# Kernel tuning notes

Hardware: AMD Instinct MI355X
Metric: run time of the kernel (lower is better)

Reference implementation:

```python
import jax, jax.numpy as jnp
import numpy as np

LEAKY_SLOPE = 0.2  # tf.nn.leaky_relu default alpha


def setup_inputs() -> dict:
    key = jax.random.key(0)
    k1, k2, k3 = jax.random.split(key, 3)
    B, T, K, D = 64, 2048, 256, 256  # batch, timesteps, n_nodes, out_dim
    inputs = jax.random.normal(k1, (B, T, K), dtype=jnp.float32)
    W = jax.random.normal(k2, (K, D), dtype=jnp.float32) * (1.0 / np.sqrt(K))
    a = jax.random.normal(k3, (2 * D, 1), dtype=jnp.float32) * (1.0 / np.sqrt(2 * D))
    return {"inputs": inputs, "W": W, "a": a}


def reference(inputs, W, a):
    # inputs: (B, T, K); W: (K, D); a: (2D, 1)
    B, T, K = inputs.shape
    D = W.shape[1]
    H = jnp.matmul(inputs, W)  # (B, T, D)
    # Original: H_concat[b,t,k] = concat([H[b,t], H[b,t]]) for every k (both
    # repeats are of the same H), so H_concat @ a == H @ (a_i + a_j), constant in k.
    a_i = a[:D, 0]
    a_j = a[D:, 0]
    e = jax.nn.leaky_relu(H @ (a_i + a_j), negative_slope=LEAKY_SLOPE)  # (B, T)
    e = jnp.broadcast_to(e[:, :, None], (B, T, K))  # (B, T, K) -- constant along K
    alpha = jax.nn.softmax(e, axis=2)  # exactly uniform 1/K
    # sum_k alpha[b,t,k] * H[b,t,d]  (H_repeat_i[b,t,k,:] == H[b,t,:])
    H_gat = jnp.einsum('btk,btd->btd', alpha, H)  # (B, T, D)
    return H_gat
```

## Files before the change

kernel.cpp:

```cpp
#include <hip/hip_runtime.h>
#include <cstdint>


static constexpr int MTOT = 64 * 2048;
static constexpr int KDIM = 256;
static constexpr int NDIM = 256;

typedef __bf16 bf16x8 __attribute__((ext_vector_type(8)));
typedef float f32x4 __attribute__((ext_vector_type(4)));

__device__ __forceinline__ uint32_t f2bf_pk(float a, float b) {
    uint32_t ua = __float_as_uint(a);
    uint32_t ub = __float_as_uint(b);
    ua = ua + 0x7fffu + ((ua >> 16) & 1u);
    ub = ub + 0x7fffu + ((ub >> 16) & 1u);
    return (ua >> 16) | (ub & 0xffff0000u);
}

__global__ void wt_transpose(const float* __restrict__ W, unsigned short* __restrict__ Wt) {
    int n = blockIdx.x;
    int k = threadIdx.x;
    float v = W[k * NDIM + n];
    uint32_t u = __float_as_uint(v);
    u = u + 0x7fffu + ((u >> 16) & 1u);
    Wt[n * KDIM + k] = (unsigned short)(u >> 16);
}

__global__ __launch_bounds__(1024, 1)
void gat_gemm(const float* __restrict__ A, const unsigned short* __restrict__ Wt,
              float* __restrict__ C) {
    __shared__ alignas(16) unsigned short Bs[128 * 256];
    __shared__ alignas(16) unsigned short As[2][256 * 64];

    const int tid  = threadIdx.x;
    const int lane = tid & 63;
    const int wave = tid >> 6;
    const int l15  = lane & 15;
    const int quad = lane >> 4;
    const int wm   = wave & 7;
    const int wn   = wave >> 3;

    const int b     = blockIdx.x;
    const int nhalf = (b >> 3) & 1;
    const int mt    = (b & 7) | ((b >> 4) << 3);
    const int bm    = mt * 256;
    const int bn    = nhalf * 128;

    const int arow = tid >> 4;
    const int acol = (tid & 15) * 4;
    const int as8  = (tid & 15) * 8;

    f32x4 acc[2][4];
#pragma unroll
    for (int i = 0; i < 2; ++i)
#pragma unroll
        for (int j = 0; j < 4; ++j)
            acc[i][j] = (f32x4)0.0f;

    auto issueA = [&](int kt, float4 (&R)[4]) {
#pragma unroll
        for (int i = 0; i < 4; ++i)
            R[i] = *(const float4*)(A + (size_t)(bm + i * 64 + arow) * KDIM + kt * 64 + acol);
    };
    auto writeA = [&](unsigned short* dst, float4 (&R)[4]) {
#pragma unroll
        for (int i = 0; i < 4; ++i) {
            const int r = i * 64 + arow;
            uint2 w;
            w.x = f2bf_pk(R[i].x, R[i].y);
            w.y = f2bf_pk(R[i].z, R[i].w);
            *(uint2*)((char*)dst + r * 128 + (as8 ^ ((r & 7) << 4))) = w;
        }
    };
    auto compute = [&](const unsigned short* asrc, int kt) {
        const char* asb = (const char*)asrc;
#pragma unroll
        for (int ks = 0; ks < 2; ++ks) {
            bf16x8 af[2];
#pragma unroll
            for (int i = 0; i < 2; ++i) {
                const int row = wm * 32 + i * 16 + l15;
                af[i] = *(const bf16x8*)(asb + row * 128 +
                          ((ks * 64 + quad * 16) ^ ((row & 7) << 4)));
            }
#pragma unroll
            for (int j = 0; j < 4; ++j) {
                const int n = wn * 64 + j * 16 + l15;
                bf16x8 bf = *(const bf16x8*)((const char*)Bs + n * 512 +
                              ((kt * 128 + ks * 64 + quad * 16) ^ ((n & 7) << 4)));
#pragma unroll
                for (int i = 0; i < 2; ++i)
                    acc[i][j] = __builtin_amdgcn_mfma_f32_16x16x32_bf16(af[i], bf, acc[i][j], 0, 0, 0);
            }
        }
    };
    auto wavebar = [&]() {
        asm volatile("s_waitcnt lgkmcnt(0)" ::: "memory");
        __builtin_amdgcn_s_barrier();
        asm volatile("" ::: "memory");
    };

    uint4 bv[4];
#pragma unroll
    for (int c = 0; c < 4; ++c) {
        const int idx = c * 1024 + tid;
        bv[c] = *(const uint4*)(Wt + (size_t)(bn + (idx >> 5)) * KDIM + (idx & 31) * 8);
    }
    float4 R0[4], R1[4];
    issueA(0, R0);
    issueA(1, R1);
#pragma unroll
    for (int c = 0; c < 4; ++c) {
        const int idx = c * 1024 + tid;
        const int n = idx >> 5, kc = idx & 31;
        *(uint4*)((char*)Bs + n * 512 + ((kc * 16) ^ ((n & 7) << 4))) = bv[c];
    }
    writeA(&As[0][0], R0);
    wavebar();

#pragma unroll
    for (int kt = 0; kt < 4; ++kt) {
        if (kt < 2) {
            if ((kt & 1) == 0) issueA(kt + 2, R0); else issueA(kt + 2, R1);
        }
        compute(&As[kt & 1][0], kt);
        if (kt < 3) {
            if ((kt & 1) == 0) writeA(&As[1][0], R1); else writeA(&As[0][0], R0);
            wavebar();
        }
    }

#pragma unroll
    for (int i = 0; i < 2; ++i) {
#pragma unroll
        for (int r = 0; r < 4; ++r) {
            const size_t row = (size_t)(bm + wm * 32 + i * 16 + quad * 4 + r);
            float* cp = C + row * NDIM + bn + wn * 64 + l15;
#pragma unroll
            for (int j = 0; j < 4; ++j)
                cp[j * 16] = acc[i][j][r];
        }
    }
}

extern "C" void kernel_launch(void* const* d_in, const int* in_sizes, int n_in,
                              void* d_out, int out_size, void* d_ws, size_t ws_size,
                              hipStream_t stream) {
    (void)in_sizes; (void)n_in; (void)out_size; (void)ws_size;
    const float* inputs = (const float*)d_in[0];
    const float* W      = (const float*)d_in[1];
    unsigned short* Wt = (unsigned short*)d_ws;
    float* out = (float*)d_out;

    hipLaunchKernelGGL(wt_transpose, dim3(NDIM), dim3(KDIM), 0, stream, W, Wt);
    hipLaunchKernelGGL(gat_gemm, dim3((MTOT / 256) * 2), dim3(1024), 0, stream, inputs, Wt, out);
}
```

Baseline: 237.0 us.

## Keep full W in LDS and stream 512 rows per block over 4 subtiles

Each block now loads the entire bf16 W (256x256) into shared memory once and loops over four 128-row M subtiles, each covering the full N width, writing results after each subtile. Before, every 256x128 tile reloaded its half of W and the A rows were read once per N half. This removes the duplicate reads of A and cuts repeated W loads. In exchange, A uses a single LDS buffer with two barriers per k-step, and the grid shrinks to 256 blocks.

```diff
diff --git a/kernel.cpp b/kernel.cpp
--- a/kernel.cpp
+++ b/kernel.cpp
@@ -29,22 +29,18 @@
 __global__ __launch_bounds__(1024, 1)
 void gat_gemm(const float* __restrict__ A, const unsigned short* __restrict__ Wt,
               float* __restrict__ C) {
-    __shared__ alignas(16) unsigned short Bs[128 * 256];
-    __shared__ alignas(16) unsigned short As[2][256 * 64];
+    __shared__ alignas(16) unsigned short Bs[256 * 256];
+    __shared__ alignas(16) unsigned short As[128 * 64];
 
     const int tid  = threadIdx.x;
     const int lane = tid & 63;
     const int wave = tid >> 6;
     const int l15  = lane & 15;
     const int quad = lane >> 4;
-    const int wm   = wave & 7;
-    const int wn   = wave >> 3;
+    const int wm   = wave & 3;
+    const int wn   = wave >> 2;
 
-    const int b     = blockIdx.x;
-    const int nhalf = (b >> 3) & 1;
-    const int mt    = (b & 7) | ((b >> 4) << 3);
-    const int bm    = mt * 256;
-    const int bn    = nhalf * 128;
+    const size_t bbase = (size_t)blockIdx.x * 512;
 
     const int arow = tid >> 4;
     const int acol = (tid & 15) * 4;
@@ -57,30 +53,27 @@
         for (int j = 0; j < 4; ++j)
             acc[i][j] = (f32x4)0.0f;
 
-    auto issueA = [&](int kt, float4 (&R)[4]) {
-#pragma unroll
-        for (int i = 0; i < 4; ++i)
-            R[i] = *(const float4*)(A + (size_t)(bm + i * 64 + arow) * KDIM + kt * 64 + acol);
+    auto issueA = [&](int s, float4 (&R)[2]) {
+        const float* ap = A + (bbase + (size_t)(s >> 2) * 128) * KDIM + (s & 3) * 64 + acol;
+        R[0] = *(const float4*)(ap + (size_t)arow * KDIM);
+        R[1] = *(const float4*)(ap + (size_t)(arow + 64) * KDIM);
     };
-    auto writeA = [&](unsigned short* dst, float4 (&R)[4]) {
-#pragma unroll
-        for (int i = 0; i < 4; ++i) {
-            const int r = i * 64 + arow;
-            uint2 w;
-            w.x = f2bf_pk(R[i].x, R[i].y);
-            w.y = f2bf_pk(R[i].z, R[i].w);
-            *(uint2*)((char*)dst + r * 128 + (as8 ^ ((r & 7) << 4))) = w;
-        }
+    auto writeA = [&](float4 (&R)[2]) {
+        uint2 w0, w1;
+        w0.x = f2bf_pk(R[0].x, R[0].y); w0.y = f2bf_pk(R[0].z, R[0].w);
+        w1.x = f2bf_pk(R[1].x, R[1].y); w1.y = f2bf_pk(R[1].z, R[1].w);
+        const int r0 = arow, r1 = arow + 64;
+        *(uint2*)((char*)As + r0 * 128 + (as8 ^ ((r0 & 7) << 4))) = w0;
+        *(uint2*)((char*)As + r1 * 128 + (as8 ^ ((r1 & 7) << 4))) = w1;
     };
-    auto compute = [&](const unsigned short* asrc, int kt) {
-        const char* asb = (const char*)asrc;
+    auto compute = [&](int kt) {
 #pragma unroll
         for (int ks = 0; ks < 2; ++ks) {
             bf16x8 af[2];
 #pragma unroll
             for (int i = 0; i < 2; ++i) {
                 const int row = wm * 32 + i * 16 + l15;
-                af[i] = *(const bf16x8*)(asb + row * 128 +
+                af[i] = *(const bf16x8*)((const char*)As + row * 128 +
                           ((ks * 64 + quad * 16) ^ ((row & 7) << 4)));
             }
 #pragma unroll
@@ -100,45 +93,54 @@
         asm volatile("" ::: "memory");
     };
 
-    uint4 bv[4];
+    uint4 bv[8];
 #pragma unroll
-    for (int c = 0; c < 4; ++c) {
+    for (int c = 0; c < 8; ++c) {
         const int idx = c * 1024 + tid;
-        bv[c] = *(const uint4*)(Wt + (size_t)(bn + (idx >> 5)) * KDIM + (idx & 31) * 8);
+        bv[c] = *(const uint4*)(Wt + (size_t)(idx >> 5) * KDIM + (idx & 31) * 8);
     }
-    float4 R0[4], R1[4];
+    float4 R0[2], R1[2];
     issueA(0, R0);
     issueA(1, R1);
 #pragma unroll
-    for (int c = 0; c < 4; ++c) {
+    for (int c = 0; c < 8; ++c) {
         const int idx = c * 1024 + tid;
         const int n = idx >> 5, kc = idx & 31;
         *(uint4*)((char*)Bs + n * 512 + ((kc * 16) ^ ((n & 7) << 4))) = bv[c];
     }
-    writeA(&As[0][0], R0);
+    writeA(R0);
     wavebar();
 
 #pragma unroll
-    for (int kt = 0; kt < 4; ++kt) {
-        if (kt < 2) {
-            if ((kt & 1) == 0) issueA(kt + 2, R0); else issueA(kt + 2, R1);
+    for (int s = 0; s < 16; ++s) {
+        if (s < 14) {
+            if (s & 1) issueA(s + 2, R1); else issueA(s + 2, R0);
         }
-        compute(&As[kt & 1][0], kt);
-        if (kt < 3) {
-            if ((kt & 1) == 0) writeA(&As[1][0], R1); else writeA(&As[0][0], R0);
+        compute(s & 3);
+
+        if ((s & 3) == 3) {
+            const size_t mb = bbase + (size_t)(s >> 2) * 128 + wm * 32;
+#pragma unroll
+            for (int i = 0; i < 2; ++i) {
+#pragma unroll
+                for (int r = 0; r < 4; ++r) {
+                    float* cp = C + (mb + i * 16 + quad * 4 + r) * NDIM + wn * 64 + l15;
+#pragma unroll
+                    for (int j = 0; j < 4; ++j)
+                        cp[j * 16] = acc[i][j][r];
+                }
+            }
+#pragma unroll
+            for (int i = 0; i < 2; ++i)
+#pragma unroll
+                for (int j = 0; j < 4; ++j)
+                    acc[i][j] = (f32x4)0.0f;
+        }
+
+        if (s < 15) {
             wavebar();
-        }
-    }
-
-#pragma unroll
-    for (int i = 0; i < 2; ++i) {
-#pragma unroll
-        for (int r = 0; r < 4; ++r) {
-            const size_t row = (size_t)(bm + wm * 32 + i * 16 + quad * 4 + r);
-            float* cp = C + row * NDIM + bn + wn * 64 + l15;
-#pragma unroll
-            for (int j = 0; j < 4; ++j)
-                cp[j * 16] = acc[i][j][r];
+            if (s & 1) writeA(R0); else writeA(R1);
+            wavebar();
         }
     }
 }
@@ -153,5 +155,5 @@
     float* out = (float*)d_out;
 
     hipLaunchKernelGGL(wt_transpose, dim3(NDIM), dim3(KDIM), 0, stream, W, Wt);
-    hipLaunchKernelGGL(gat_gemm, dim3((MTOT / 256) * 2), dim3(1024), 0, stream, inputs, Wt, out);
+    hipLaunchKernelGGL(gat_gemm, dim3(MTOT / 512), dim3(1024), 0, stream, inputs, Wt, out);
 }
```

New measurement: 250.2 us. 1.06x slower.
